# Kernel tuning notes

Measured on AMD Instinct MI355X. Metric: run time of the kernel, lower is better.

The kernel has to match this reference:

```python
import jax, jax.numpy as jnp
import numpy as np

H = 256   # hidden_dim
NH = 8    # attention heads, embed_dim = 2*H

def _ln(x, g, b, eps=1e-5):
    m = x.mean(-1, keepdims=True)
    v = ((x - m) ** 2).mean(-1, keepdims=True)
    return (x - m) / jnp.sqrt(v + eps) * g + b


def setup_inputs() -> dict:
    key = jax.random.key(0)
    ks = jax.random.split(key, 16)
    B, T, R, P = 32, 2048, 16, 2
    E = 2 * H
    s = 0.02
    n = lambda k, shp: (jax.random.normal(k, shp, jnp.float32) * s)
    z = lambda shp: jnp.zeros(shp, jnp.float32)
    return {
        "encoded_tasks": jax.random.normal(ks[0], (B, T, E), jnp.float32),
        "context": jax.random.normal(ks[1], (B, H), jnp.float32),
        "preference": jax.random.uniform(ks[2], (B, P), dtype=jnp.float32),
        "pref_W": n(ks[3], (P, H)), "pref_b": z((H,)),
        "ln_g": jnp.ones((H,), jnp.float32), "ln_b": z((H,)),
        "Wq": n(ks[4], (E, E)), "bq": z((E,)),
        "Wk": n(ks[5], (E, E)), "bk": z((E,)),
        "Wv": n(ks[6], (E, E)), "bv": z((E,)),
        "Wo": n(ks[7], (E, E)), "bo": z((E,)),
        "W_ih": n(ks[8], (4 * H, 3 * H)), "b_ih": z((4 * H,)),
        "W_hh": n(ks[9], (4 * H, H)), "b_hh": z((4 * H,)),
        "hW1": n(ks[10], (3 * H, H)), "hb1": z((H,)),
        "hW2": n(ks[11], (H, R)), "hb2": z((R,)),
        "num_steps": 32,
    }


def reference(encoded_tasks, context, preference, pref_W, pref_b, ln_g, ln_b,
              Wq, bq, Wk, bk, Wv, bv, Wo, bo,
              W_ih, b_ih, W_hh, b_hh, hW1, hb1, hW2, hb2, num_steps):
    B, T, E = encoded_tasks.shape
    Dh = E // NH
    scale = 1.0 / jnp.sqrt(jnp.float32(Dh))
    # preference encoder: Linear -> ReLU -> LayerNorm
    pref = _ln(jax.nn.relu(preference @ pref_W + pref_b), ln_g, ln_b)  # [B, H]
    # K/V projections of encoded_tasks are step-invariant: compute once
    K = (encoded_tasks @ Wk + bk).reshape(B, T, NH, Dh)
    V = (encoded_tasks @ Wv + bv).reshape(B, T, NH, Dh)
    h0 = context[:, :H]
    c0 = jnp.zeros_like(h0)

    def step(carry, _):
        h, c = carry
        q = jnp.concatenate([h, pref], axis=-1)              # [B, 2H]
        qh = (q @ Wq + bq).reshape(B, NH, Dh) * scale
        scores = jnp.einsum('bhd,bthd->bht', qh, K)
        w = jax.nn.softmax(scores, axis=-1)
        attn = jnp.einsum('bht,bthd->bhd', w, V).reshape(B, E)
        ctx = attn @ Wo + bo                                  # [B, 2H]
        x = jnp.concatenate([h, ctx[:, :H], pref], axis=-1)   # [B, 3H]
        gates = x @ W_ih.T + b_ih + h @ W_hh.T + b_hh         # [B, 4H]
        i, f, g, o = jnp.split(gates, 4, axis=-1)
        c_new = jax.nn.sigmoid(f) * c + jax.nn.sigmoid(i) * jnp.tanh(g)
        h_new = jax.nn.sigmoid(o) * jnp.tanh(c_new)
        dec = jnp.concatenate([h_new, ctx[:, :H], pref], axis=-1)
        logits = jax.nn.relu(dec @ hW1 + hb1) @ hW2 + hb2     # [B, R]
        return (h_new, c_new), logits

    (_, _), logits = jax.lax.scan(step, (h0, c0), None, length=num_steps)
    return jnp.transpose(logits, (1, 0, 2))  # [B, num_steps, R]
```

## Files before the change

kernel.cpp:

```cpp
#include <hip/hip_runtime.h>
#include <hip/hip_bf16.h>


typedef __bf16 bf16;
typedef __attribute__((ext_vector_type(8))) __bf16 bf16x8;
typedef __attribute__((ext_vector_type(4))) __bf16 bf16x4;
typedef __attribute__((ext_vector_type(4))) float f32x4;

#define B_  32
#define T_  2048
#define H_  256
#define S_  32

static __device__ __forceinline__ float sigmoidf_(float x){ return 1.f/(1.f+__expf(-x)); }
static __device__ __forceinline__ float tanhf_(float x){ float e=__expf(2.f*x); return (e-1.f)/(e+1.f); }

#define NX4_ 8388608
__global__ void prep_misc(const float* __restrict__ X,
                          const float* __restrict__ Wq, const float* __restrict__ Wk,
                          const float* __restrict__ Wv, const float* __restrict__ Wo,
                          const float* __restrict__ Wih, const float* __restrict__ Whh,
                          const float* __restrict__ context,
                          bf16* __restrict__ Xb,
                          bf16* __restrict__ WkvT, bf16* __restrict__ WqT, bf16* __restrict__ WoT,
                          bf16* __restrict__ WihB, bf16* __restrict__ WhhB,
                          float* __restrict__ h0, float* __restrict__ c0, float* __restrict__ ctxz)
{
  const int scalar_total = 524288+262144+131072+786432+262144+8192+8192+262144;
  const int total = NX4_ + scalar_total;
  for (int i = blockIdx.x*blockDim.x + threadIdx.x; i < total; i += gridDim.x*blockDim.x){
    if (i < NX4_){
      float4 x4 = *(const float4*)&X[(size_t)i*4];
      bf16x4 o; o[0]=(bf16)x4.x; o[1]=(bf16)x4.y; o[2]=(bf16)x4.z; o[3]=(bf16)x4.w;
      *(bf16x4*)&Xb[(size_t)i*4] = o;
      continue;
    }
    int x = i - NX4_;
    if (x < 524288){ int n = x>>9, k = x&511;
      WkvT[x] = (bf16)(n<512 ? Wk[k*512+n] : Wv[k*512+(n-512)]); continue; }
    x -= 524288;
    if (x < 262144){ int n = x>>9, k = x&511; WqT[x] = (bf16)Wq[k*512+n]; continue; }
    x -= 262144;
    if (x < 131072){ int h = x>>14, rem = x&16383, j = rem>>6, d = rem&63;
      WoT[x] = (bf16)Wo[(h*64+d)*512 + j]; continue; }
    x -= 131072;
    if (x < 786432){ WihB[x] = (bf16)Wih[x]; continue; }
    x -= 786432;
    if (x < 262144){ WhhB[x] = (bf16)Whh[x]; continue; }
    x -= 262144;
    if (x < 8192){ h0[x] = context[x]; continue; }
    x -= 8192;
    if (x < 8192){ c0[x] = 0.f; continue; }
    x -= 8192;
    ctxz[x] = 0.f;
  }
}

__global__ __launch_bounds__(256) void prep_pref(const float* __restrict__ preference,
                                                 const float* __restrict__ pref_W,
                                                 const float* __restrict__ pref_b,
                                                 const float* __restrict__ ln_g,
                                                 const float* __restrict__ ln_b,
                                                 float* __restrict__ prefb)
{
  __shared__ float red_[4];
  int b = blockIdx.x, j = threadIdx.x;
  float p0 = preference[b*2], p1 = preference[b*2+1];
  float v = fmaxf(p0*pref_W[j] + p1*pref_W[256+j] + pref_b[j], 0.f);
  float s = v;
  #pragma unroll
  for (int o=32;o;o>>=1) s += __shfl_xor(s,o);
  if ((j&63)==0) red_[j>>6] = s;
  __syncthreads();
  float mean = (red_[0]+red_[1]+red_[2]+red_[3]) * (1.f/256.f);
  __syncthreads();
  float d = v - mean;
  float s2 = d*d;
  #pragma unroll
  for (int o=32;o;o>>=1) s2 += __shfl_xor(s2,o);
  if ((j&63)==0) red_[j>>6] = s2;
  __syncthreads();
  float var = (red_[0]+red_[1]+red_[2]+red_[3]) * (1.f/256.f);
  prefb[b*256+j] = d * rsqrtf(var + 1e-5f) * ln_g[j] + ln_b[j];
}

__global__ __launch_bounds__(256) void gemm_kv(const bf16* __restrict__ Xb,
                                               const bf16* __restrict__ WkvT,
                                               const float* __restrict__ bk, const float* __restrict__ bv,
                                               bf16* __restrict__ Kp, bf16* __restrict__ Vp)
{
  __shared__ __align__(16) bf16 As[128*40];
  __shared__ __align__(16) bf16 Bs[128*40];
  int blk = blockIdx.x;
  int bm = blk>>3, bn = blk&7;
  int m0 = bm<<7, n0 = bn<<7;
  int tid = threadIdx.x;
  int lane = tid&63, wave = tid>>6;
  int wm = (wave>>1)<<6, wn = (wave&1)<<6;
  int q = lane>>4, li = lane&15;
  f32x4 acc[4][4];
  #pragma unroll
  for (int a=0;a<4;a++)
    #pragma unroll
    for (int b=0;b<4;b++) acc[a][b] = (f32x4){0.f,0.f,0.f,0.f};

  for (int k0=0;k0<512;k0+=32){
    __syncthreads();
    #pragma unroll
    for (int it=0;it<2;it++){
      int chunk = it*256+tid;
      int r = chunk>>2, oct = chunk&3;
      *(bf16x8*)&As[r*40+oct*8] = *(const bf16x8*)&Xb[(size_t)(m0+r)*512 + k0 + oct*8];
      *(bf16x8*)&Bs[r*40+oct*8] = *(const bf16x8*)&WkvT[(size_t)(n0+r)*512 + k0 + oct*8];
    }
    __syncthreads();
    bf16x8 af[4], bfr[4];
    #pragma unroll
    for (int mt=0;mt<4;mt++) af[mt] = *(const bf16x8*)&As[(wm+mt*16+li)*40 + q*8];
    #pragma unroll
    for (int nt=0;nt<4;nt++) bfr[nt] = *(const bf16x8*)&Bs[(wn+nt*16+li)*40 + q*8];
    #pragma unroll
    for (int mt=0;mt<4;mt++)
      #pragma unroll
      for (int nt=0;nt<4;nt++)
        acc[mt][nt] = __builtin_amdgcn_mfma_f32_16x16x32_bf16(bfr[nt], af[mt], acc[mt][nt], 0,0,0);
  }
  #pragma unroll
  for (int mt=0;mt<4;mt++){
    int mm = m0 + wm + mt*16 + li;
    int b = mm>>11, t = mm&2047;
    #pragma unroll
    for (int nt=0;nt<4;nt++){
      int nb = n0 + wn + nt*16 + q*4;
      const float* bias = (nb<512) ? (bk+nb) : (bv+nb-512);
      bf16* dst = (nb<512) ? Kp : Vp;
      int nn = nb & 511;
      int h = nn>>6, d0 = nn&63;
      bf16x4 o4;
      #pragma unroll
      for (int r=0;r<4;r++) o4[r] = (bf16)(acc[mt][nt][r] + bias[r]);
      *(bf16x4*)&dst[(((size_t)(b*8+h))*T_ + (size_t)t)*64 + d0] = o4;
    }
  }
}

__global__ __launch_bounds__(1024) void attn_step(const bf16* __restrict__ Kp, const bf16* __restrict__ Vp,
                                                  const bf16* __restrict__ WqT, const bf16* __restrict__ WoT,
                                                  const float* __restrict__ bq, const float* __restrict__ prefb,
                                                  const float* __restrict__ h_prev, float* __restrict__ ctx_s)
{
  __shared__ float q_s[512];
  __shared__ float qh_s[64];
  __shared__ float aw[16][64];
  __shared__ float zw[16];
  __shared__ float attn_s[64];
  int b = blockIdx.x>>3, h = blockIdx.x&7;
  int tid = threadIdx.x;
  if (tid < 512) q_s[tid] = (tid<256) ? h_prev[b*256+tid] : prefb[b*256+(tid-256)];
  __syncthreads();
  {
    int d = tid>>4, p = tid&15;
    const bf16* wr = &WqT[(size_t)(h*64+d)*512 + p*32];
    const float* qq = &q_s[p*32];
    float s = 0.f;
    #pragma unroll
    for (int i=0;i<4;i++){
      bf16x8 w8 = *(const bf16x8*)&wr[i*8];
      #pragma unroll
      for (int j=0;j<8;j++) s += qq[i*8+j]*(float)w8[j];
    }
    s += __shfl_xor(s,1); s += __shfl_xor(s,2); s += __shfl_xor(s,4); s += __shfl_xor(s,8);
    if (p==0) qh_s[d] = (s + bq[h*64+d])*0.125f;
  }
  __syncthreads();
  int lane = tid&63, wave = tid>>6;
  int ro = lane>>3, doct = lane&7;
  float qhf[8];
  #pragma unroll
  for (int j=0;j<8;j++) qhf[j] = qh_s[doct*8+j];
  const bf16* Kb = Kp + ((size_t)(b*8+h))*T_*64;
  const bf16* Vb = Vp + ((size_t)(b*8+h))*T_*64;
  float acc[8];
  #pragma unroll
  for (int j=0;j<8;j++) acc[j]=0.f;
  float z = 0.f;
  #pragma unroll 4
  for (int it=0; it<16; ++it){
    int t = it*128 + wave*8 + ro;
    bf16x8 k8 = *(const bf16x8*)&Kb[(size_t)t*64 + doct*8];
    bf16x8 v8 = *(const bf16x8*)&Vb[(size_t)t*64 + doct*8];
    float s = 0.f;
    #pragma unroll
    for (int j=0;j<8;j++) s += qhf[j]*(float)k8[j];
    s += __shfl_xor(s,1); s += __shfl_xor(s,2); s += __shfl_xor(s,4);
    float e = __expf(fminf(s, 80.f));
    z += e;
    #pragma unroll
    for (int j=0;j<8;j++) acc[j] += e*(float)v8[j];
  }
  #pragma unroll
  for (int j=0;j<8;j++){
    acc[j] += __shfl_xor(acc[j],8);
    acc[j] += __shfl_xor(acc[j],16);
    acc[j] += __shfl_xor(acc[j],32);
  }
  z += __shfl_xor(z,8); z += __shfl_xor(z,16); z += __shfl_xor(z,32);
  if (lane<8){
    #pragma unroll
    for (int j=0;j<8;j++) aw[wave][lane*8+j] = acc[j];
    if (lane==0) zw[wave] = z;
  }
  __syncthreads();
  if (tid < 64){
    float Z = 0.f, a = 0.f;
    #pragma unroll
    for (int w=0;w<16;w++){ Z += zw[w]; a += aw[w][tid]; }
    attn_s[tid] = a / Z;
  }
  __syncthreads();
  {
    int j = tid>>2, p4 = tid&3;
    const bf16* wo = &WoT[(((size_t)h*256)+j)*64 + p4*16];
    const float* at = &attn_s[p4*16];
    float cp = 0.f;
    #pragma unroll
    for (int i=0;i<2;i++){
      bf16x8 w8 = *(const bf16x8*)&wo[i*8];
      #pragma unroll
      for (int u=0;u<8;u++) cp += at[i*8+u]*(float)w8[u];
    }
    cp += __shfl_xor(cp,1); cp += __shfl_xor(cp,2);
    if (p4==0) atomicAdd(&ctx_s[b*256+j], cp);
  }
}

__global__ __launch_bounds__(256) void gates_lstm(const float* __restrict__ h_prev, const float* __restrict__ ctx_s,
                                                  const float* __restrict__ prefb, const float* __restrict__ bo,
                                                  const bf16* __restrict__ WihB, const bf16* __restrict__ WhhB,
                                                  const float* __restrict__ b_ih, const float* __restrict__ b_hh,
                                                  const float* __restrict__ c_prev,
                                                  float* __restrict__ c_out, float* __restrict__ h_out)
{
  __shared__ __align__(16) bf16 xs[32*1032];
  __shared__ float gsum[2][32][18];
  int bk = blockIdx.x;
  int tid = threadIdx.x;
  #pragma unroll
  for (int i=0;i<32;i++){
    int u = i*256 + tid;
    int bb = u>>8, kq = u&255;
    int k = kq*4;
    float v0,v1,v2,v3;
    if (k < 256){
      const float* p = &h_prev[bb*256+k];
      v0=p[0];v1=p[1];v2=p[2];v3=p[3];
    } else if (k < 512){
      int j2 = k-256;
      const float* p = &ctx_s[bb*256+j2];
      v0=p[0]+bo[j2]; v1=p[1]+bo[j2+1]; v2=p[2]+bo[j2+2]; v3=p[3]+bo[j2+3];
    } else if (k < 768){
      const float* p = &prefb[bb*256+(k-512)];
      v0=p[0];v1=p[1];v2=p[2];v3=p[3];
    } else {
      const float* p = &h_prev[bb*256+(k-768)];
      v0=p[0];v1=p[1];v2=p[2];v3=p[3];
    }
    bf16x4 w4; w4[0]=(bf16)v0; w4[1]=(bf16)v1; w4[2]=(bf16)v2; w4[3]=(bf16)v3;
    *(bf16x4*)&xs[bb*1032+k] = w4;
  }
  __syncthreads();
  int lane = tid&63, wave = tid>>6;
  int q = lane>>4, li = lane&15;
  int mt = wave&1, kh = wave>>1;
  int g = li>>2, jj = li&3;
  int n = g*256 + bk*4 + jj;
  f32x4 acc = (f32x4){0.f,0.f,0.f,0.f};
  #pragma unroll 4
  for (int kk = kh*512; kk < kh*512+512; kk += 32){
    bf16x8 af = *(const bf16x8*)&xs[(mt*16+li)*1032 + kk + q*8];
    int kg = kk + q*8;
    const bf16* wp = (kg<768) ? &WihB[(size_t)n*768 + kg] : &WhhB[(size_t)n*256 + (kg-768)];
    bf16x8 bfrag = *(const bf16x8*)wp;
    acc = __builtin_amdgcn_mfma_f32_16x16x32_bf16(af, bfrag, acc, 0,0,0);
  }
  #pragma unroll
  for (int r=0;r<4;r++) gsum[kh][mt*16 + q*4 + r][li] = acc[r];
  __syncthreads();
  if (tid < 128){
    int b2 = tid>>2, j2 = tid&3;
    float val[4];
    #pragma unroll
    for (int gg=0; gg<4; gg++){
      int ng = gg*256 + bk*4 + j2;
      val[gg] = gsum[0][b2][gg*4+j2] + gsum[1][b2][gg*4+j2] + b_ih[ng] + b_hh[ng];
    }
    int J = bk*4 + j2;
    float cp = c_prev[b2*256+J];
    float cn = sigmoidf_(val[1])*cp + sigmoidf_(val[0])*tanhf_(val[2]);
    float hn = sigmoidf_(val[3])*tanhf_(cn);
    c_out[b2*256+J] = cn;
    h_out[b2*256+J] = hn;
  }
}

__global__ __launch_bounds__(256) void epilogue_k(const float* __restrict__ h_hist, const float* __restrict__ ctx_all,
                                                  const float* __restrict__ bo,
                                                  const float* __restrict__ prefb, const float* __restrict__ hW1,
                                                  const float* __restrict__ hb1, const float* __restrict__ hW2,
                                                  const float* __restrict__ hb2, float* __restrict__ out)
{
  __shared__ float dec[8][768];
  __shared__ float hid[8][260];
  int blk = blockIdx.x;
  int tid = threadIdx.x;
  #pragma unroll
  for (int i=0;i<8;i++){
    int sb = blk*8+i;
    int s = sb>>5, b = sb&31;
    for (int k=tid; k<768; k+=256){
      float v;
      if (k<256)      v = h_hist[((size_t)(s+1)*32 + b)*256 + k];
      else if (k<512) v = ctx_all[((size_t)s*32 + b)*256 + (k-256)] + bo[k-256];
      else            v = prefb[b*256 + (k-512)];
      dec[i][k] = v;
    }
  }
  __syncthreads();
  float a[8];
  #pragma unroll
  for (int i=0;i<8;i++) a[i]=0.f;
  for (int k=0;k<768;k++){
    float w = hW1[(size_t)k*256 + tid];
    #pragma unroll
    for (int i=0;i<8;i++) a[i] += dec[i][k]*w;
  }
  float b1 = hb1[tid];
  #pragma unroll
  for (int i=0;i<8;i++) hid[i][tid] = fmaxf(a[i]+b1, 0.f);
  __syncthreads();
  if (tid < 128){
    int i = tid>>4, r = tid&15;
    float s2 = 0.f;
    for (int j2=0;j2<256;j2++) s2 += hid[i][j2]*hW2[j2*16+r];
    s2 += hb2[r];
    int sb = blk*8+i;
    int st = sb>>5, b = sb&31;
    out[(size_t)b*512 + st*16 + r] = s2;
  }
}

extern "C" void kernel_launch(void* const* d_in, const int* in_sizes, int n_in,
                              void* d_out, int out_size, void* d_ws, size_t ws_size,
                              hipStream_t stream)
{
  const float* X          = (const float*)d_in[0];
  const float* context    = (const float*)d_in[1];
  const float* preference = (const float*)d_in[2];
  const float* pref_W     = (const float*)d_in[3];
  const float* pref_b     = (const float*)d_in[4];
  const float* ln_g       = (const float*)d_in[5];
  const float* ln_b       = (const float*)d_in[6];
  const float* Wq         = (const float*)d_in[7];
  const float* bq         = (const float*)d_in[8];
  const float* Wk         = (const float*)d_in[9];
  const float* bk         = (const float*)d_in[10];
  const float* Wv         = (const float*)d_in[11];
  const float* bv         = (const float*)d_in[12];
  const float* Wo         = (const float*)d_in[13];
  const float* bo         = (const float*)d_in[14];
  const float* W_ih       = (const float*)d_in[15];
  const float* b_ih       = (const float*)d_in[16];
  const float* W_hh       = (const float*)d_in[17];
  const float* b_hh       = (const float*)d_in[18];
  const float* hW1        = (const float*)d_in[19];
  const float* hb1        = (const float*)d_in[20];
  const float* hW2        = (const float*)d_in[21];
  const float* hb2        = (const float*)d_in[22];
  float* out = (float*)d_out;

  char* ws = (char*)d_ws;
  size_t off = 0;
  auto alloc = [&](size_t bytes)->char*{ char* p = ws+off; off += (bytes+255)&~(size_t)255; return p; };
  bf16* Xb      = (bf16*)alloc((size_t)B_*T_*512*2);
  bf16* Kp      = (bf16*)alloc((size_t)B_*8*T_*64*2);
  bf16* Vp      = (bf16*)alloc((size_t)B_*8*T_*64*2);
  bf16* WkvT    = (bf16*)alloc(1024ull*512*2);
  bf16* WqT     = (bf16*)alloc(512ull*512*2);
  bf16* WoT     = (bf16*)alloc(8ull*256*64*2);
  bf16* WihB    = (bf16*)alloc(1024ull*768*2);
  bf16* WhhB    = (bf16*)alloc(1024ull*256*2);
  float* prefb  = (float*)alloc(8192ull*4);
  float* h_hist = (float*)alloc(33ull*8192*4);
  float* c_hist = (float*)alloc(33ull*8192*4);
  float* ctx_all= (float*)alloc(32ull*8192*4);
  (void)ws_size; (void)in_sizes; (void)n_in; (void)out_size;

  hipLaunchKernelGGL(prep_misc, dim3(2048), dim3(256), 0, stream,
                     X, Wq,Wk,Wv,Wo,W_ih,W_hh,context,
                     Xb, WkvT,WqT,WoT,WihB,WhhB, h_hist, c_hist, ctx_all);
  hipLaunchKernelGGL(prep_pref, dim3(32), dim3(256), 0, stream,
                     preference, pref_W, pref_b, ln_g, ln_b, prefb);
  hipLaunchKernelGGL(gemm_kv, dim3(4096), dim3(256), 0, stream, Xb, WkvT, bk, bv, Kp, Vp);
  for (int s=0;s<S_;s++){
    hipLaunchKernelGGL(attn_step, dim3(256), dim3(1024), 0, stream,
                       Kp, Vp, WqT, WoT, bq, prefb,
                       h_hist + (size_t)s*8192, ctx_all + (size_t)s*8192);
    hipLaunchKernelGGL(gates_lstm, dim3(64), dim3(256), 0, stream,
                       h_hist + (size_t)s*8192, ctx_all + (size_t)s*8192,
                       prefb, bo, WihB, WhhB, b_ih, b_hh,
                       c_hist + (size_t)s*8192,
                       c_hist + (size_t)(s+1)*8192, h_hist + (size_t)(s+1)*8192);
  }
  hipLaunchKernelGGL(epilogue_k, dim3(128), dim3(256), 0, stream,
                     h_hist, ctx_all, bo, prefb, hW1, hb1, hW2, hb2, out);
}
```

Before: 1.679 ms.

## Store K/V in FP8, fuse X bf16 conversion into GEMM with register prefetch

K and V projections are now written as FP8 (e4m3 via cvt_pk_fp8) instead of bf16, which halves the bytes the 32 attention steps stream from memory. The attention loop is reworked so each lane handles 16 dims of a row using packed FP8-to-f32 conversions. The separate X-to-bf16 conversion pass and its buffer are removed: gemm_kv reads fp32 X directly, converts while staging into shared memory, and prefetches the next k-tile into registers. The block index mapping is also reordered so that consecutive blocks cover different M tiles. FP8 storage of K/V lowers attention precision and may push the result past the accuracy tolerance.

After: 1.730 ms. 1.03x slower.

```diff
diff --git a/kernel.cpp b/kernel.cpp
--- a/kernel.cpp
+++ b/kernel.cpp
@@ -6,6 +6,7 @@
 typedef __attribute__((ext_vector_type(8))) __bf16 bf16x8;
 typedef __attribute__((ext_vector_type(4))) __bf16 bf16x4;
 typedef __attribute__((ext_vector_type(4))) float f32x4;
+typedef __attribute__((ext_vector_type(2))) float f32x2;
 
 #define B_  32
 #define T_  2048
@@ -15,27 +16,17 @@
 static __device__ __forceinline__ float sigmoidf_(float x){ return 1.f/(1.f+__expf(-x)); }
 static __device__ __forceinline__ float tanhf_(float x){ float e=__expf(2.f*x); return (e-1.f)/(e+1.f); }
 
-#define NX4_ 8388608
-__global__ void prep_misc(const float* __restrict__ X,
-                          const float* __restrict__ Wq, const float* __restrict__ Wk,
+__global__ void prep_misc(const float* __restrict__ Wq, const float* __restrict__ Wk,
                           const float* __restrict__ Wv, const float* __restrict__ Wo,
                           const float* __restrict__ Wih, const float* __restrict__ Whh,
                           const float* __restrict__ context,
-                          bf16* __restrict__ Xb,
                           bf16* __restrict__ WkvT, bf16* __restrict__ WqT, bf16* __restrict__ WoT,
                           bf16* __restrict__ WihB, bf16* __restrict__ WhhB,
                           float* __restrict__ h0, float* __restrict__ c0, float* __restrict__ ctxz)
 {
-  const int scalar_total = 524288+262144+131072+786432+262144+8192+8192+262144;
-  const int total = NX4_ + scalar_total;
+  const int total = 524288+262144+131072+786432+262144+8192+8192+262144;
   for (int i = blockIdx.x*blockDim.x + threadIdx.x; i < total; i += gridDim.x*blockDim.x){
-    if (i < NX4_){
-      float4 x4 = *(const float4*)&X[(size_t)i*4];
-      bf16x4 o; o[0]=(bf16)x4.x; o[1]=(bf16)x4.y; o[2]=(bf16)x4.z; o[3]=(bf16)x4.w;
-      *(bf16x4*)&Xb[(size_t)i*4] = o;
-      continue;
-    }
-    int x = i - NX4_;
+    int x = i;
     if (x < 524288){ int n = x>>9, k = x&511;
       WkvT[x] = (bf16)(n<512 ? Wk[k*512+n] : Wv[k*512+(n-512)]); continue; }
     x -= 524288;
@@ -84,36 +75,52 @@
   prefb[b*256+j] = d * rsqrtf(var + 1e-5f) * ln_g[j] + ln_b[j];
 }
 
-__global__ __launch_bounds__(256) void gemm_kv(const bf16* __restrict__ Xb,
+__global__ __launch_bounds__(256) void gemm_kv(const float* __restrict__ X,
                                                const bf16* __restrict__ WkvT,
                                                const float* __restrict__ bk, const float* __restrict__ bv,
-                                               bf16* __restrict__ Kp, bf16* __restrict__ Vp)
+                                               unsigned char* __restrict__ Kf8, unsigned char* __restrict__ Vf8)
 {
   __shared__ __align__(16) bf16 As[128*40];
   __shared__ __align__(16) bf16 Bs[128*40];
   int blk = blockIdx.x;
-  int bm = blk>>3, bn = blk&7;
+  int bm = ((blk>>6)<<3) | (blk&7);
+  int bn = (blk>>3)&7;
   int m0 = bm<<7, n0 = bn<<7;
   int tid = threadIdx.x;
   int lane = tid&63, wave = tid>>6;
   int wm = (wave>>1)<<6, wn = (wave&1)<<6;
   int q = lane>>4, li = lane&15;
+  int r = tid>>1, half = tid&1;
+  const float* Xrow = &X[(size_t)(m0+r)*512 + half*16];
+  const bf16*  Brow = &WkvT[(size_t)(n0+r)*512 + half*16];
   f32x4 acc[4][4];
   #pragma unroll
   for (int a=0;a<4;a++)
     #pragma unroll
     for (int b=0;b<4;b++) acc[a][b] = (f32x4){0.f,0.f,0.f,0.f};
+
+  float4 apf[4]; bf16x8 bpf[2];
+  #pragma unroll
+  for (int i=0;i<4;i++) apf[i] = *(const float4*)(Xrow + i*4);
+  bpf[0] = *(const bf16x8*)(Brow);
+  bpf[1] = *(const bf16x8*)(Brow + 8);
 
   for (int k0=0;k0<512;k0+=32){
     __syncthreads();
     #pragma unroll
-    for (int it=0;it<2;it++){
-      int chunk = it*256+tid;
-      int r = chunk>>2, oct = chunk&3;
-      *(bf16x8*)&As[r*40+oct*8] = *(const bf16x8*)&Xb[(size_t)(m0+r)*512 + k0 + oct*8];
-      *(bf16x8*)&Bs[r*40+oct*8] = *(const bf16x8*)&WkvT[(size_t)(n0+r)*512 + k0 + oct*8];
-    }
+    for (int i=0;i<4;i++){
+      bf16x4 a4; a4[0]=(bf16)apf[i].x; a4[1]=(bf16)apf[i].y; a4[2]=(bf16)apf[i].z; a4[3]=(bf16)apf[i].w;
+      *(bf16x4*)&As[r*40 + half*16 + i*4] = a4;
+    }
+    *(bf16x8*)&Bs[r*40 + half*16]     = bpf[0];
+    *(bf16x8*)&Bs[r*40 + half*16 + 8] = bpf[1];
     __syncthreads();
+    if (k0+32 < 512){
+      #pragma unroll
+      for (int i=0;i<4;i++) apf[i] = *(const float4*)(Xrow + k0+32 + i*4);
+      bpf[0] = *(const bf16x8*)(Brow + k0+32);
+      bpf[1] = *(const bf16x8*)(Brow + k0+40);
+    }
     bf16x8 af[4], bfr[4];
     #pragma unroll
     for (int mt=0;mt<4;mt++) af[mt] = *(const bf16x8*)&As[(wm+mt*16+li)*40 + q*8];
@@ -133,18 +140,19 @@
     for (int nt=0;nt<4;nt++){
       int nb = n0 + wn + nt*16 + q*4;
       const float* bias = (nb<512) ? (bk+nb) : (bv+nb-512);
-      bf16* dst = (nb<512) ? Kp : Vp;
+      unsigned char* dst = (nb<512) ? Kf8 : Vf8;
       int nn = nb & 511;
       int h = nn>>6, d0 = nn&63;
-      bf16x4 o4;
-      #pragma unroll
-      for (int r=0;r<4;r++) o4[r] = (bf16)(acc[mt][nt][r] + bias[r]);
-      *(bf16x4*)&dst[(((size_t)(b*8+h))*T_ + (size_t)t)*64 + d0] = o4;
-    }
-  }
-}
-
-__global__ __launch_bounds__(1024) void attn_step(const bf16* __restrict__ Kp, const bf16* __restrict__ Vp,
+      unsigned int p = 0;
+      p = __builtin_amdgcn_cvt_pk_fp8_f32(acc[mt][nt][0]+bias[0], acc[mt][nt][1]+bias[1], p, false);
+      p = __builtin_amdgcn_cvt_pk_fp8_f32(acc[mt][nt][2]+bias[2], acc[mt][nt][3]+bias[3], p, true);
+      *(unsigned int*)&dst[(((size_t)(b*8+h))*T_ + (size_t)t)*64 + d0] = p;
+    }
+  }
+}
+
+__global__ __launch_bounds__(1024) void attn_step(const unsigned char* __restrict__ Kf8,
+                                                  const unsigned char* __restrict__ Vf8,
                                                   const bf16* __restrict__ WqT, const bf16* __restrict__ WoT,
                                                   const float* __restrict__ bq, const float* __restrict__ prefb,
                                                   const float* __restrict__ h_prev, float* __restrict__ ctx_s)
@@ -174,41 +182,58 @@
   }
   __syncthreads();
   int lane = tid&63, wave = tid>>6;
-  int ro = lane>>3, doct = lane&7;
-  float qhf[8];
-  #pragma unroll
-  for (int j=0;j<8;j++) qhf[j] = qh_s[doct*8+j];
-  const bf16* Kb = Kp + ((size_t)(b*8+h))*T_*64;
-  const bf16* Vb = Vp + ((size_t)(b*8+h))*T_*64;
-  float acc[8];
-  #pragma unroll
-  for (int j=0;j<8;j++) acc[j]=0.f;
+  int ro = lane>>2, dq = lane&3;
+  float qhf[16];
+  #pragma unroll
+  for (int j=0;j<16;j++) qhf[j] = qh_s[dq*16+j];
+  const unsigned char* Kb = Kf8 + ((size_t)(b*8+h))*T_*64;
+  const unsigned char* Vb = Vf8 + ((size_t)(b*8+h))*T_*64;
+  float acc[16];
+  #pragma unroll
+  for (int j=0;j<16;j++) acc[j]=0.f;
   float z = 0.f;
-  #pragma unroll 4
-  for (int it=0; it<16; ++it){
-    int t = it*128 + wave*8 + ro;
-    bf16x8 k8 = *(const bf16x8*)&Kb[(size_t)t*64 + doct*8];
-    bf16x8 v8 = *(const bf16x8*)&Vb[(size_t)t*64 + doct*8];
+  #pragma unroll
+  for (int it=0; it<8; ++it){
+    int t = it*256 + wave*16 + ro;
+    uint4 k4 = *(const uint4*)&Kb[(size_t)t*64 + dq*16];
+    uint4 v4 = *(const uint4*)&Vb[(size_t)t*64 + dq*16];
     float s = 0.f;
-    #pragma unroll
-    for (int j=0;j<8;j++) s += qhf[j]*(float)k8[j];
-    s += __shfl_xor(s,1); s += __shfl_xor(s,2); s += __shfl_xor(s,4);
+    { f32x2 t0, t1;
+      t0 = __builtin_amdgcn_cvt_pk_f32_fp8(k4.x,false); t1 = __builtin_amdgcn_cvt_pk_f32_fp8(k4.x,true);
+      s += qhf[0]*t0.x + qhf[1]*t0.y + qhf[2]*t1.x + qhf[3]*t1.y;
+      t0 = __builtin_amdgcn_cvt_pk_f32_fp8(k4.y,false); t1 = __builtin_amdgcn_cvt_pk_f32_fp8(k4.y,true);
+      s += qhf[4]*t0.x + qhf[5]*t0.y + qhf[6]*t1.x + qhf[7]*t1.y;
+      t0 = __builtin_amdgcn_cvt_pk_f32_fp8(k4.z,false); t1 = __builtin_amdgcn_cvt_pk_f32_fp8(k4.z,true);
+      s += qhf[8]*t0.x + qhf[9]*t0.y + qhf[10]*t1.x + qhf[11]*t1.y;
+      t0 = __builtin_amdgcn_cvt_pk_f32_fp8(k4.w,false); t1 = __builtin_amdgcn_cvt_pk_f32_fp8(k4.w,true);
+      s += qhf[12]*t0.x + qhf[13]*t0.y + qhf[14]*t1.x + qhf[15]*t1.y;
+    }
+    s += __shfl_xor(s,1); s += __shfl_xor(s,2);
     float e = __expf(fminf(s, 80.f));
     z += e;
-    #pragma unroll
-    for (int j=0;j<8;j++) acc[j] += e*(float)v8[j];
-  }
-  #pragma unroll
-  for (int j=0;j<8;j++){
+    { f32x2 t0, t1;
+      t0 = __builtin_amdgcn_cvt_pk_f32_fp8(v4.x,false); t1 = __builtin_amdgcn_cvt_pk_f32_fp8(v4.x,true);
+      acc[0]+=e*t0.x; acc[1]+=e*t0.y; acc[2]+=e*t1.x; acc[3]+=e*t1.y;
+      t0 = __builtin_amdgcn_cvt_pk_f32_fp8(v4.y,false); t1 = __builtin_amdgcn_cvt_pk_f32_fp8(v4.y,true);
+      acc[4]+=e*t0.x; acc[5]+=e*t0.y; acc[6]+=e*t1.x; acc[7]+=e*t1.y;
+      t0 = __builtin_amdgcn_cvt_pk_f32_fp8(v4.z,false); t1 = __builtin_amdgcn_cvt_pk_f32_fp8(v4.z,true);
+      acc[8]+=e*t0.x; acc[9]+=e*t0.y; acc[10]+=e*t1.x; acc[11]+=e*t1.y;
+      t0 = __builtin_amdgcn_cvt_pk_f32_fp8(v4.w,false); t1 = __builtin_amdgcn_cvt_pk_f32_fp8(v4.w,true);
+      acc[12]+=e*t0.x; acc[13]+=e*t0.y; acc[14]+=e*t1.x; acc[15]+=e*t1.y;
+    }
+  }
+  #pragma unroll
+  for (int j=0;j<16;j++){
+    acc[j] += __shfl_xor(acc[j],4);
     acc[j] += __shfl_xor(acc[j],8);
     acc[j] += __shfl_xor(acc[j],16);
     acc[j] += __shfl_xor(acc[j],32);
   }
-  z += __shfl_xor(z,8); z += __shfl_xor(z,16); z += __shfl_xor(z,32);
-  if (lane<8){
-    #pragma unroll
-    for (int j=0;j<8;j++) aw[wave][lane*8+j] = acc[j];
-    if (lane==0) zw[wave] = z;
+  z += __shfl_xor(z,4); z += __shfl_xor(z,8); z += __shfl_xor(z,16); z += __shfl_xor(z,32);
+  if (ro==0){
+    #pragma unroll
+    for (int j=0;j<16;j++) aw[wave][dq*16+j] = acc[j];
+    if (dq==0) zw[wave] = z;
   }
   __syncthreads();
   if (tid < 64){
@@ -272,8 +297,7 @@
   int lane = tid&63, wave = tid>>6;
   int q = lane>>4, li = lane&15;
   int mt = wave&1, kh = wave>>1;
-  int g = li>>2, jj = li&3;
-  int n = g*256 + bk*4 + jj;
+  int n = (li>>2)*256 + bk*4 + (li&3);
   f32x4 acc = (f32x4){0.f,0.f,0.f,0.f};
   #pragma unroll 4
   for (int kk = kh*512; kk < kh*512+512; kk += 32){
@@ -381,9 +405,8 @@
   char* ws = (char*)d_ws;
   size_t off = 0;
   auto alloc = [&](size_t bytes)->char*{ char* p = ws+off; off += (bytes+255)&~(size_t)255; return p; };
-  bf16* Xb      = (bf16*)alloc((size_t)B_*T_*512*2);
-  bf16* Kp      = (bf16*)alloc((size_t)B_*8*T_*64*2);
-  bf16* Vp      = (bf16*)alloc((size_t)B_*8*T_*64*2);
+  unsigned char* Kf8 = (unsigned char*)alloc((size_t)B_*8*T_*64);
+  unsigned char* Vf8 = (unsigned char*)alloc((size_t)B_*8*T_*64);
   bf16* WkvT    = (bf16*)alloc(1024ull*512*2);
   bf16* WqT     = (bf16*)alloc(512ull*512*2);
   bf16* WoT     = (bf16*)alloc(8ull*256*64*2);
@@ -395,15 +418,15 @@
   float* ctx_all= (float*)alloc(32ull*8192*4);
   (void)ws_size; (void)in_sizes; (void)n_in; (void)out_size;
 
-  hipLaunchKernelGGL(prep_misc, dim3(2048), dim3(256), 0, stream,
-                     X, Wq,Wk,Wv,Wo,W_ih,W_hh,context,
-                     Xb, WkvT,WqT,WoT,WihB,WhhB, h_hist, c_hist, ctx_all);
+  hipLaunchKernelGGL(prep_misc, dim3(512), dim3(256), 0, stream,
+                     Wq,Wk,Wv,Wo,W_ih,W_hh,context,
+                     WkvT,WqT,WoT,WihB,WhhB, h_hist, c_hist, ctx_all);
   hipLaunchKernelGGL(prep_pref, dim3(32), dim3(256), 0, stream,
                      preference, pref_W, pref_b, ln_g, ln_b, prefb);
-  hipLaunchKernelGGL(gemm_kv, dim3(4096), dim3(256), 0, stream, Xb, WkvT, bk, bv, Kp, Vp);
+  hipLaunchKernelGGL(gemm_kv, dim3(4096), dim3(256), 0, stream, X, WkvT, bk, bv, Kf8, Vf8);
   for (int s=0;s<S_;s++){
     hipLaunchKernelGGL(attn_step, dim3(256), dim3(1024), 0, stream,
-                       Kp, Vp, WqT, WoT, bq, prefb,
+                       Kf8, Vf8, WqT, WoT, bq, prefb,
                        h_hist + (size_t)s*8192, ctx_all + (size_t)s*8192);
     hipLaunchKernelGGL(gates_lstm, dim3(64), dim3(256), 0, stream,
                        h_hist + (size_t)s*8192, ctx_all + (size_t)s*8192,
```
